# Optimization experiments

Measured on AMD Instinct MI355X. Metric: run time of the kernel, lower is better.

## Reference

```python
import jax, jax.numpy as jnp
import numpy as np

G, N, D, H = 2, 192, 64, 4
DK = D // H


def setup_inputs() -> dict:
    key = jax.random.key(0)
    ks = jax.random.split(key, 9)
    s = 0.05
    return {
        "adj": jax.random.normal(ks[0], (G, N, N, D), dtype=jnp.float32),
        "Wq": jax.random.normal(ks[1], (D, D), dtype=jnp.float32) * s,
        "bq": jax.random.normal(ks[2], (D,), dtype=jnp.float32) * s,
        "Wk": jax.random.normal(ks[3], (D, D), dtype=jnp.float32) * s,
        "bk": jax.random.normal(ks[4], (D,), dtype=jnp.float32) * s,
        "Wv": jax.random.normal(ks[5], (D, D), dtype=jnp.float32) * s,
        "bv": jax.random.normal(ks[6], (D,), dtype=jnp.float32) * s,
        "Wo": jax.random.normal(ks[7], (D, D), dtype=jnp.float32) * s,
        "bo": jax.random.normal(ks[8], (D,), dtype=jnp.float32) * s,
    }


def _proj_heads(x, W, b):
    # x: (G,N,N,D) -> (G,N,H,N,DK); W stored as (in,out)
    y = jnp.einsum('gnmd,de->gnme', x, W) + b
    g, n, m, _ = y.shape
    return y.reshape(g, n, m, H, DK).transpose(0, 1, 3, 2, 4)


def reference(adj, Wq, bq, Wk, bk, Wv, bv, Wo, bo):
    q = _proj_heads(adj, Wq, bq)  # (G,N,H,N,DK)
    k = _proj_heads(adj, Wk, bk)
    v = _proj_heads(adj, Wv, bv)
    scores = jnp.einsum('gnhtd,gnhsd->gnhts', q, k) / jnp.sqrt(jnp.float32(DK))
    p = jax.nn.softmax(scores, axis=-1)  # (G,N,H,N,N)
    x = jnp.einsum('gnhts,gnhsd->gnhtd', p, v)  # (G,N,H,N,DK)
    x = x.transpose(0, 1, 3, 2, 4).reshape(adj.shape[0], adj.shape[1], -1, H * DK)
    return jnp.einsum('gnmd,de->gnme', x, Wo) + bo
```

## Files before the change

### kernel.cpp

```cpp
#include <hip/hip_runtime.h>


typedef float    f32x4 __attribute__((ext_vector_type(4)));
typedef _Float16 f16x4 __attribute__((ext_vector_type(4)));
typedef _Float16 f16x8 __attribute__((ext_vector_type(8)));

__device__ __forceinline__ int xsw64(int r, int c) {
    return (r << 6) + (((c >> 3) ^ (r & 7)) << 3) + (c & 7);
}
__device__ __forceinline__ int vsw192(int r, int c) {
    return r * 192 + ((((c >> 3) ^ (r & 7)) & 31) << 3) + (c & 7);
}

extern "C" __global__ void __launch_bounds__(512, 4)
spa_mfma2(const float* __restrict__ adj,
          const float* __restrict__ Wq, const float* __restrict__ bq,
          const float* __restrict__ Wk, const float* __restrict__ bk,
          const float* __restrict__ Wv, const float* __restrict__ bv,
          const float* __restrict__ Wo, const float* __restrict__ bo,
          float* __restrict__ out) {
    extern __shared__ __align__(16) char smem[];
    _Float16* X  = (_Float16*)smem;
    _Float16* VT = (_Float16*)smem + 12288;
    _Float16* WT = (_Float16*)smem + 24576;

    const int tid = threadIdx.x;
    const int l   = tid & 63;
    const int wv  = tid >> 6;
    const int l15 = l & 15;
    const int g   = l >> 4;

    const float* Xg   = adj + (size_t)blockIdx.x * (192 * 64);
    float*       outg = out + (size_t)blockIdx.x * (192 * 64);

    {
        const int d0 = (tid & 7) << 3;
        const int t0 = tid >> 3;
        for (int p = 0; p < 3; ++p) {
            int t = t0 + (p << 6);
            const float4* src = (const float4*)&Xg[(t << 6) + d0];
            float4 v0 = src[0], v1 = src[1];
            f16x8 h8;
            h8[0]=(_Float16)v0.x; h8[1]=(_Float16)v0.y; h8[2]=(_Float16)v0.z; h8[3]=(_Float16)v0.w;
            h8[4]=(_Float16)v1.x; h8[5]=(_Float16)v1.y; h8[6]=(_Float16)v1.z; h8[7]=(_Float16)v1.w;
            *(f16x8*)&X[xsw64(t, d0)] = h8;
        }
    }
    {
        const int e  = tid & 63;
        const int db = (tid >> 6) << 3;
        const float* Ws[4] = {Wq, Wk, Wv, Wo};
#pragma unroll
        for (int m = 0; m < 4; ++m) {
            f16x8 h8;
#pragma unroll
            for (int j = 0; j < 8; ++j) h8[j] = (_Float16)Ws[m][(db + j) * 64 + e];
            *(f16x8*)&WT[m * 4096 + xsw64(e, db)] = h8;
        }
    }
    __syncthreads();

    const f32x4 z = {0.f, 0.f, 0.f, 0.f};
    const int h  = wv >> 1;
    const int eh = h << 4;

    {
        const int et  = wv & 3;
        const int stb = (wv >> 2) * 6;
        f16x8 w0 = *(const f16x8*)&WT[2*4096 + xsw64((et<<4)+l15, g<<3)];
        f16x8 w1 = *(const f16x8*)&WT[2*4096 + xsw64((et<<4)+l15, 32+(g<<3))];
        f32x4 b4 = *(const f32x4*)&bv[(et<<4)+(g<<2)];
        for (int s6 = 0; s6 < 6; ++s6) {
            int st = stb + s6;
            f16x8 x0 = *(const f16x8*)&X[xsw64((st<<4)+l15, g<<3)];
            f16x8 x1 = *(const f16x8*)&X[xsw64((st<<4)+l15, 32+(g<<3))];
            f32x4 c = __builtin_amdgcn_mfma_f32_16x16x32_f16(w0, x0, z, 0,0,0);
            c = __builtin_amdgcn_mfma_f32_16x16x32_f16(w1, x1, c, 0,0,0);
            int s = (st << 4) + l15;
#pragma unroll
            for (int r = 0; r < 4; ++r)
                VT[vsw192((et<<4)+(g<<2)+r, s)] = (_Float16)(c[r] + b4[r]);
        }
    }

    f16x4 kf[12];
    {
        f16x8 w0 = *(const f16x8*)&WT[1*4096 + xsw64(eh+l15, g<<3)];
        f16x8 w1 = *(const f16x8*)&WT[1*4096 + xsw64(eh+l15, 32+(g<<3))];
        f32x4 b4 = *(const f32x4*)&bk[eh+(g<<2)];
#pragma unroll
        for (int st = 0; st < 12; ++st) {
            f16x8 x0 = *(const f16x8*)&X[xsw64((st<<4)+l15, g<<3)];
            f16x8 x1 = *(const f16x8*)&X[xsw64((st<<4)+l15, 32+(g<<3))];
            f32x4 c = __builtin_amdgcn_mfma_f32_16x16x32_f16(w0, x0, z, 0,0,0);
            c = __builtin_amdgcn_mfma_f32_16x16x32_f16(w1, x1, c, 0,0,0);
#pragma unroll
            for (int r = 0; r < 4; ++r) kf[st][r] = (_Float16)(c[r] + b4[r]);
        }
    }

    f16x4 qf[6];
    const int ttb = (wv & 1) * 6;
    {
        f16x8 w0 = *(const f16x8*)&WT[0*4096 + xsw64(eh+l15, g<<3)];
        f16x8 w1 = *(const f16x8*)&WT[0*4096 + xsw64(eh+l15, 32+(g<<3))];
        f32x4 b4 = *(const f32x4*)&bq[eh+(g<<2)];
        const float qs = 0.25f * 1.4426950408889634f;
#pragma unroll
        for (int j = 0; j < 6; ++j) {
            int tt = ttb + j;
            f16x8 x0 = *(const f16x8*)&X[xsw64((tt<<4)+l15, g<<3)];
            f16x8 x1 = *(const f16x8*)&X[xsw64((tt<<4)+l15, 32+(g<<3))];
            f32x4 c = __builtin_amdgcn_mfma_f32_16x16x32_f16(w0, x0, z, 0,0,0);
            c = __builtin_amdgcn_mfma_f32_16x16x32_f16(w1, x1, c, 0,0,0);
#pragma unroll
            for (int r = 0; r < 4; ++r) qf[j][r] = (_Float16)((c[r] + b4[r]) * qs);
        }
    }
    __syncthreads();

    f16x4 vf[12];
#pragma unroll
    for (int st = 0; st < 12; ++st)
        vf[st] = *(const f16x4*)&VT[vsw192(eh+l15, (st<<4)+(g<<2))];

    for (int j = 0; j < 6; ++j) {
        f32x4 accA = z, accB = z;
        float rsum = 0.f;
#pragma unroll
        for (int st = 0; st < 12; ++st) {
            f32x4 c = __builtin_amdgcn_mfma_f32_16x16x16f16(kf[st], qf[j], z, 0,0,0);
            float p0 = exp2f(c[0]), p1 = exp2f(c[1]);
            float p2 = exp2f(c[2]), p3 = exp2f(c[3]);
            rsum += (p0 + p1) + (p2 + p3);
            f16x4 pf;
            pf[0]=(_Float16)p0; pf[1]=(_Float16)p1; pf[2]=(_Float16)p2; pf[3]=(_Float16)p3;
            if (st & 1) accB = __builtin_amdgcn_mfma_f32_16x16x16f16(vf[st], pf, accB, 0,0,0);
            else        accA = __builtin_amdgcn_mfma_f32_16x16x16f16(vf[st], pf, accA, 0,0,0);
        }
        rsum += __shfl_xor(rsum, 16);
        rsum += __shfl_xor(rsum, 32);
        const float rinv = 1.0f / rsum;
        f16x4 o4;
#pragma unroll
        for (int r = 0; r < 4; ++r) o4[r] = (_Float16)((accA[r] + accB[r]) * rinv);
        *(f16x4*)&X[xsw64(((ttb + j) << 4) + l15, eh + (g << 2))] = o4;
    }
    __syncthreads();

    {
        const int eo = ((wv & 3) << 4) + l15;
        f16x8 w0 = *(const f16x8*)&WT[3*4096 + xsw64(eo, g<<3)];
        f16x8 w1 = *(const f16x8*)&WT[3*4096 + xsw64(eo, 32+(g<<3))];
        const float bov = bo[eo];
#pragma unroll
        for (int i = 0; i < 6; ++i) {
            int tt = (wv + (i << 3)) >> 2;
            f16x8 a0 = *(const f16x8*)&X[xsw64((tt<<4)+l15, g<<3)];
            f16x8 a1 = *(const f16x8*)&X[xsw64((tt<<4)+l15, 32+(g<<3))];
            f32x4 c = __builtin_amdgcn_mfma_f32_16x16x32_f16(a0, w0, z, 0,0,0);
            c = __builtin_amdgcn_mfma_f32_16x16x32_f16(a1, w1, c, 0,0,0);
#pragma unroll
            for (int r = 0; r < 4; ++r)
                outg[(((tt << 4) + (g << 2) + r) << 6) + eo] = c[r] + bov;
        }
    }
}

extern "C" void kernel_launch(void* const* d_in, const int* in_sizes, int n_in,
                              void* d_out, int out_size, void* d_ws, size_t ws_size,
                              hipStream_t stream) {
    (void)in_sizes; (void)n_in; (void)d_ws; (void)ws_size; (void)out_size;
    const float* adj = (const float*)d_in[0];
    const float* Wq  = (const float*)d_in[1];
    const float* bq  = (const float*)d_in[2];
    const float* Wk  = (const float*)d_in[3];
    const float* bk  = (const float*)d_in[4];
    const float* Wv  = (const float*)d_in[5];
    const float* bv  = (const float*)d_in[6];
    const float* Wo  = (const float*)d_in[7];
    const float* bo  = (const float*)d_in[8];
    float* out = (float*)d_out;

    const int shmem = 81920;
    hipFuncSetAttribute((const void*)spa_mfma2,
                        hipFuncAttributeMaxDynamicSharedMemorySize, shmem);
    spa_mfma2<<<2 * 192, 512, shmem, stream>>>(adj, Wq, bq, Wk, bk, Wv, bv, Wo, bo, out);
}
```

Before: 110.4 us.

## Split each graph row across two blocks and precompute fp16 weights in prep kernel

Adds a small prep kernel that converts the four weight matrices to fp16 (folding the softmax scale into Wq/bq) in workspace, removing per-block weight transposition and its LDS storage. The main kernel now launches two blocks per (g,n), each handling half of the query tiles, with reduced shared memory and a higher occupancy hint. Probability packing uses cvt_pkrtz. In exchange, each half block re-reads adj and recomputes the full K and V projections, doubling that traffic and work.

```diff
diff --git a/kernel.cpp b/kernel.cpp
--- a/kernel.cpp
+++ b/kernel.cpp
@@ -2,6 +2,8 @@
 
 
 typedef float    f32x4 __attribute__((ext_vector_type(4)));
+typedef float    f32x2 __attribute__((ext_vector_type(2)));
+typedef _Float16 f16x2 __attribute__((ext_vector_type(2)));
 typedef _Float16 f16x4 __attribute__((ext_vector_type(4)));
 typedef _Float16 f16x8 __attribute__((ext_vector_type(8)));
 
@@ -12,30 +14,68 @@
     return r * 192 + ((((c >> 3) ^ (r & 7)) & 31) << 3) + (c & 7);
 }
 
-extern "C" __global__ void __launch_bounds__(512, 4)
-spa_mfma2(const float* __restrict__ adj,
-          const float* __restrict__ Wq, const float* __restrict__ bq,
-          const float* __restrict__ Wk, const float* __restrict__ bk,
-          const float* __restrict__ Wv, const float* __restrict__ bv,
-          const float* __restrict__ Wo, const float* __restrict__ bo,
+#define QSCALE 0.36067376022224085f
+
+extern "C" __global__ void spa_prep(const float* __restrict__ Wq, const float* __restrict__ bq,
+                                    const float* __restrict__ Wk, const float* __restrict__ bk,
+                                    const float* __restrict__ Wv, const float* __restrict__ bv,
+                                    const float* __restrict__ Wo, const float* __restrict__ bo,
+                                    _Float16* __restrict__ WT, float* __restrict__ BS) {
+    const int t = blockIdx.x * 256 + threadIdx.x;
+    const int m  = t >> 10;
+    const int e  = (t >> 4) & 63;
+    const int d0 = (t & 15) << 2;
+    const float* W[4] = {Wq, Wk, Wv, Wo};
+    const float s = (m == 0) ? QSCALE : 1.0f;
+    f16x4 h4;
+#pragma unroll
+    for (int j = 0; j < 4; ++j) h4[j] = (_Float16)(W[m][(d0 + j) * 64 + e] * s);
+    *(f16x4*)&WT[(m << 12) + (e << 6) + d0] = h4;
+    if (t < 256) {
+        const int mm = t >> 6, ee = t & 63;
+        const float* B[4] = {bq, bk, bv, bo};
+        BS[t] = B[mm][ee] * ((mm == 0) ? QSCALE : 1.0f);
+    }
+}
+
+extern "C" __global__ void __launch_bounds__(512, 6)
+spa_mfma3(const float* __restrict__ adj,
+          const _Float16* __restrict__ WTg, const float* __restrict__ BS,
           float* __restrict__ out) {
     extern __shared__ __align__(16) char smem[];
     _Float16* X  = (_Float16*)smem;
     _Float16* VT = (_Float16*)smem + 12288;
-    _Float16* WT = (_Float16*)smem + 24576;
 
-    const int tid = threadIdx.x;
-    const int l   = tid & 63;
-    const int wv  = tid >> 6;
-    const int l15 = l & 15;
-    const int g   = l >> 4;
+    const int tid  = threadIdx.x;
+    const int l    = tid & 63;
+    const int wv   = tid >> 6;
+    const int l15  = l & 15;
+    const int g    = l >> 4;
+    const int gn   = blockIdx.x >> 1;
+    const int half = blockIdx.x & 1;
+    const int ttb  = half * 6;
 
-    const float* Xg   = adj + (size_t)blockIdx.x * (192 * 64);
-    float*       outg = out + (size_t)blockIdx.x * (192 * 64);
+    const float* Xg   = adj + (size_t)gn * (192 * 64);
+    float*       outg = out + (size_t)gn * (192 * 64);
+
+    const int h  = wv >> 1;
+    const int eh = h << 4;
+    const int et = wv & 3;
+
+    const f16x8 wv0 = *(const f16x8*)&WTg[(2 << 12) + (((et << 4) + l15) << 6) + (g << 3)];
+    const f16x8 wv1 = *(const f16x8*)&WTg[(2 << 12) + (((et << 4) + l15) << 6) + 32 + (g << 3)];
+    const f16x8 wk0 = *(const f16x8*)&WTg[(1 << 12) + ((eh + l15) << 6) + (g << 3)];
+    const f16x8 wk1 = *(const f16x8*)&WTg[(1 << 12) + ((eh + l15) << 6) + 32 + (g << 3)];
+    const f16x8 wq0 = *(const f16x8*)&WTg[(0 << 12) + ((eh + l15) << 6) + (g << 3)];
+    const f16x8 wq1 = *(const f16x8*)&WTg[(0 << 12) + ((eh + l15) << 6) + 32 + (g << 3)];
+    const f32x4 bv4 = *(const f32x4*)&BS[128 + (et << 4) + (g << 2)];
+    const f32x4 bk4 = *(const f32x4*)&BS[64 + eh + (g << 2)];
+    const f32x4 bq4 = *(const f32x4*)&BS[0 + eh + (g << 2)];
 
     {
         const int d0 = (tid & 7) << 3;
         const int t0 = tid >> 3;
+#pragma unroll
         for (int p = 0; p < 3; ++p) {
             int t = t0 + (p << 6);
             const float4* src = (const float4*)&Xg[(t << 6) + d0];
@@ -46,120 +86,93 @@
             *(f16x8*)&X[xsw64(t, d0)] = h8;
         }
     }
-    {
-        const int e  = tid & 63;
-        const int db = (tid >> 6) << 3;
-        const float* Ws[4] = {Wq, Wk, Wv, Wo};
-#pragma unroll
-        for (int m = 0; m < 4; ++m) {
-            f16x8 h8;
-#pragma unroll
-            for (int j = 0; j < 8; ++j) h8[j] = (_Float16)Ws[m][(db + j) * 64 + e];
-            *(f16x8*)&WT[m * 4096 + xsw64(e, db)] = h8;
-        }
-    }
     __syncthreads();
 
     const f32x4 z = {0.f, 0.f, 0.f, 0.f};
-    const int h  = wv >> 1;
-    const int eh = h << 4;
 
     {
-        const int et  = wv & 3;
         const int stb = (wv >> 2) * 6;
-        f16x8 w0 = *(const f16x8*)&WT[2*4096 + xsw64((et<<4)+l15, g<<3)];
-        f16x8 w1 = *(const f16x8*)&WT[2*4096 + xsw64((et<<4)+l15, 32+(g<<3))];
-        f32x4 b4 = *(const f32x4*)&bv[(et<<4)+(g<<2)];
         for (int s6 = 0; s6 < 6; ++s6) {
             int st = stb + s6;
-            f16x8 x0 = *(const f16x8*)&X[xsw64((st<<4)+l15, g<<3)];
-            f16x8 x1 = *(const f16x8*)&X[xsw64((st<<4)+l15, 32+(g<<3))];
-            f32x4 c = __builtin_amdgcn_mfma_f32_16x16x32_f16(w0, x0, z, 0,0,0);
-            c = __builtin_amdgcn_mfma_f32_16x16x32_f16(w1, x1, c, 0,0,0);
+            f16x8 x0 = *(const f16x8*)&X[xsw64((st << 4) + l15, g << 3)];
+            f16x8 x1 = *(const f16x8*)&X[xsw64((st << 4) + l15, 32 + (g << 3))];
+            f32x4 c = __builtin_amdgcn_mfma_f32_16x16x32_f16(wv0, x0, z, 0, 0, 0);
+            c = __builtin_amdgcn_mfma_f32_16x16x32_f16(wv1, x1, c, 0, 0, 0);
             int s = (st << 4) + l15;
 #pragma unroll
             for (int r = 0; r < 4; ++r)
-                VT[vsw192((et<<4)+(g<<2)+r, s)] = (_Float16)(c[r] + b4[r]);
+                VT[vsw192((et << 4) + (g << 2) + r, s)] = (_Float16)(c[r] + bv4[r]);
         }
     }
 
     f16x4 kf[12];
-    {
-        f16x8 w0 = *(const f16x8*)&WT[1*4096 + xsw64(eh+l15, g<<3)];
-        f16x8 w1 = *(const f16x8*)&WT[1*4096 + xsw64(eh+l15, 32+(g<<3))];
-        f32x4 b4 = *(const f32x4*)&bk[eh+(g<<2)];
 #pragma unroll
-        for (int st = 0; st < 12; ++st) {
-            f16x8 x0 = *(const f16x8*)&X[xsw64((st<<4)+l15, g<<3)];
-            f16x8 x1 = *(const f16x8*)&X[xsw64((st<<4)+l15, 32+(g<<3))];
-            f32x4 c = __builtin_amdgcn_mfma_f32_16x16x32_f16(w0, x0, z, 0,0,0);
-            c = __builtin_amdgcn_mfma_f32_16x16x32_f16(w1, x1, c, 0,0,0);
+    for (int st = 0; st < 12; ++st) {
+        f16x8 x0 = *(const f16x8*)&X[xsw64((st << 4) + l15, g << 3)];
+        f16x8 x1 = *(const f16x8*)&X[xsw64((st << 4) + l15, 32 + (g << 3))];
+        f32x4 c = __builtin_amdgcn_mfma_f32_16x16x32_f16(wk0, x0, z, 0, 0, 0);
+        c = __builtin_amdgcn_mfma_f32_16x16x32_f16(wk1, x1, c, 0, 0, 0);
 #pragma unroll
-            for (int r = 0; r < 4; ++r) kf[st][r] = (_Float16)(c[r] + b4[r]);
-        }
+        for (int r = 0; r < 4; ++r) kf[st][r] = (_Float16)(c[r] + bk4[r]);
     }
 
-    f16x4 qf[6];
-    const int ttb = (wv & 1) * 6;
-    {
-        f16x8 w0 = *(const f16x8*)&WT[0*4096 + xsw64(eh+l15, g<<3)];
-        f16x8 w1 = *(const f16x8*)&WT[0*4096 + xsw64(eh+l15, 32+(g<<3))];
-        f32x4 b4 = *(const f32x4*)&bq[eh+(g<<2)];
-        const float qs = 0.25f * 1.4426950408889634f;
+    f16x4 qf[3];
+    const int tloc = (wv & 1) * 3;
 #pragma unroll
-        for (int j = 0; j < 6; ++j) {
-            int tt = ttb + j;
-            f16x8 x0 = *(const f16x8*)&X[xsw64((tt<<4)+l15, g<<3)];
-            f16x8 x1 = *(const f16x8*)&X[xsw64((tt<<4)+l15, 32+(g<<3))];
-            f32x4 c = __builtin_amdgcn_mfma_f32_16x16x32_f16(w0, x0, z, 0,0,0);
-            c = __builtin_amdgcn_mfma_f32_16x16x32_f16(w1, x1, c, 0,0,0);
+    for (int j = 0; j < 3; ++j) {
+        int tt = ttb + tloc + j;
+        f16x8 x0 = *(const f16x8*)&X[xsw64((tt << 4) + l15, g << 3)];
+        f16x8 x1 = *(const f16x8*)&X[xsw64((tt << 4) + l15, 32 + (g << 3))];
+        f32x4 c = __builtin_amdgcn_mfma_f32_16x16x32_f16(wq0, x0, z, 0, 0, 0);
+        c = __builtin_amdgcn_mfma_f32_16x16x32_f16(wq1, x1, c, 0, 0, 0);
 #pragma unroll
-            for (int r = 0; r < 4; ++r) qf[j][r] = (_Float16)((c[r] + b4[r]) * qs);
-        }
+        for (int r = 0; r < 4; ++r) qf[j][r] = (_Float16)(c[r] + bq4[r]);
     }
     __syncthreads();
 
     f16x4 vf[12];
 #pragma unroll
     for (int st = 0; st < 12; ++st)
-        vf[st] = *(const f16x4*)&VT[vsw192(eh+l15, (st<<4)+(g<<2))];
+        vf[st] = *(const f16x4*)&VT[vsw192(eh + l15, (st << 4) + (g << 2))];
 
-    for (int j = 0; j < 6; ++j) {
+    for (int j = 0; j < 3; ++j) {
         f32x4 accA = z, accB = z;
-        float rsum = 0.f;
+        f32x2 rs = {0.f, 0.f};
 #pragma unroll
         for (int st = 0; st < 12; ++st) {
-            f32x4 c = __builtin_amdgcn_mfma_f32_16x16x16f16(kf[st], qf[j], z, 0,0,0);
+            f32x4 c = __builtin_amdgcn_mfma_f32_16x16x16f16(kf[st], qf[j], z, 0, 0, 0);
             float p0 = exp2f(c[0]), p1 = exp2f(c[1]);
             float p2 = exp2f(c[2]), p3 = exp2f(c[3]);
-            rsum += (p0 + p1) + (p2 + p3);
-            f16x4 pf;
-            pf[0]=(_Float16)p0; pf[1]=(_Float16)p1; pf[2]=(_Float16)p2; pf[3]=(_Float16)p3;
-            if (st & 1) accB = __builtin_amdgcn_mfma_f32_16x16x16f16(vf[st], pf, accB, 0,0,0);
-            else        accA = __builtin_amdgcn_mfma_f32_16x16x16f16(vf[st], pf, accA, 0,0,0);
+            rs += (f32x2){p0, p1} + (f32x2){p2, p3};
+            f16x2 lo = __builtin_bit_cast(f16x2, __builtin_amdgcn_cvt_pkrtz(p0, p1));
+            f16x2 hi = __builtin_bit_cast(f16x2, __builtin_amdgcn_cvt_pkrtz(p2, p3));
+            f16x4 pf = __builtin_shufflevector(lo, hi, 0, 1, 2, 3);
+            if (st & 1) accB = __builtin_amdgcn_mfma_f32_16x16x16f16(vf[st], pf, accB, 0, 0, 0);
+            else        accA = __builtin_amdgcn_mfma_f32_16x16x16f16(vf[st], pf, accA, 0, 0, 0);
         }
+        float rsum = rs[0] + rs[1];
         rsum += __shfl_xor(rsum, 16);
         rsum += __shfl_xor(rsum, 32);
         const float rinv = 1.0f / rsum;
         f16x4 o4;
 #pragma unroll
         for (int r = 0; r < 4; ++r) o4[r] = (_Float16)((accA[r] + accB[r]) * rinv);
-        *(f16x4*)&X[xsw64(((ttb + j) << 4) + l15, eh + (g << 2))] = o4;
+        *(f16x4*)&X[xsw64(((ttb + tloc + j) << 4) + l15, eh + (g << 2))] = o4;
     }
     __syncthreads();
 
     {
         const int eo = ((wv & 3) << 4) + l15;
-        f16x8 w0 = *(const f16x8*)&WT[3*4096 + xsw64(eo, g<<3)];
-        f16x8 w1 = *(const f16x8*)&WT[3*4096 + xsw64(eo, 32+(g<<3))];
-        const float bov = bo[eo];
+        const f16x8 wo0 = *(const f16x8*)&WTg[(3 << 12) + (eo << 6) + (g << 3)];
+        const f16x8 wo1 = *(const f16x8*)&WTg[(3 << 12) + (eo << 6) + 32 + (g << 3)];
+        const float bov = BS[192 + eo];
 #pragma unroll
-        for (int i = 0; i < 6; ++i) {
-            int tt = (wv + (i << 3)) >> 2;
-            f16x8 a0 = *(const f16x8*)&X[xsw64((tt<<4)+l15, g<<3)];
-            f16x8 a1 = *(const f16x8*)&X[xsw64((tt<<4)+l15, 32+(g<<3))];
-            f32x4 c = __builtin_amdgcn_mfma_f32_16x16x32_f16(a0, w0, z, 0,0,0);
-            c = __builtin_amdgcn_mfma_f32_16x16x32_f16(a1, w1, c, 0,0,0);
+        for (int i = 0; i < 3; ++i) {
+            int tt = ttb + ((wv + (i << 3)) >> 2);
+            f16x8 a0 = *(const f16x8*)&X[xsw64((tt << 4) + l15, g << 3)];
+            f16x8 a1 = *(const f16x8*)&X[xsw64((tt << 4) + l15, 32 + (g << 3))];
+            f32x4 c = __builtin_amdgcn_mfma_f32_16x16x32_f16(a0, wo0, z, 0, 0, 0);
+            c = __builtin_amdgcn_mfma_f32_16x16x32_f16(a1, wo1, c, 0, 0, 0);
 #pragma unroll
             for (int r = 0; r < 4; ++r)
                 outg[(((tt << 4) + (g << 2) + r) << 6) + eo] = c[r] + bov;
@@ -170,20 +183,17 @@
 extern "C" void kernel_launch(void* const* d_in, const int* in_sizes, int n_in,
                               void* d_out, int out_size, void* d_ws, size_t ws_size,
                               hipStream_t stream) {
-    (void)in_sizes; (void)n_in; (void)d_ws; (void)ws_size; (void)out_size;
+    (void)in_sizes; (void)n_in; (void)ws_size; (void)out_size;
     const float* adj = (const float*)d_in[0];
-    const float* Wq  = (const float*)d_in[1];
-    const float* bq  = (const float*)d_in[2];
-    const float* Wk  = (const float*)d_in[3];
-    const float* bk  = (const float*)d_in[4];
-    const float* Wv  = (const float*)d_in[5];
-    const float* bv  = (const float*)d_in[6];
-    const float* Wo  = (const float*)d_in[7];
-    const float* bo  = (const float*)d_in[8];
-    float* out = (float*)d_out;
+    _Float16* WT = (_Float16*)d_ws;
+    float*    BS = (float*)((char*)d_ws + 32768);
 
-    const int shmem = 81920;
-    hipFuncSetAttribute((const void*)spa_mfma2,
-                        hipFuncAttributeMaxDynamicSharedMemorySize, shmem);
-    spa_mfma2<<<2 * 192, 512, shmem, stream>>>(adj, Wq, bq, Wk, bk, Wv, bv, Wo, bo, out);
+    spa_prep<<<16, 256, 0, stream>>>((const float*)d_in[1], (const float*)d_in[2],
+                                     (const float*)d_in[3], (const float*)d_in[4],
+                                     (const float*)d_in[5], (const float*)d_in[6],
+                                     (const float*)d_in[7], (const float*)d_in[8],
+                                     WT, BS);
+
+    const int shmem = 49152;
+    spa_mfma3<<<2 * 192 * 2, 512, shmem, stream>>>(adj, WT, BS, (float*)d_out);
 }
```

Result: slower. 118.9 us (+7.8%).
